# Kernel tuning notes

Measured on AMD Instinct MI355X. Metric: run time of the kernel, lower is better.

The kernel has to match this reference:

```python
import jax, jax.numpy as jnp
import numpy as np

B, N, SEM, STR = 64, 512, 256, 256  # batch, tokens, sem_dim_size, str_dim_size (hidden=512)


def setup_inputs() -> dict:
    key = jax.random.key(0)
    ks = jax.random.split(key, 8)
    s = 0.02  # small init so exp(f_ij)/exp(f_i) stay well-conditioned
    return {
        "input": jax.random.normal(ks[0], (B, N, SEM + STR), jnp.float32),
        "Wp": (jax.random.normal(ks[1], (STR, STR), jnp.float32) * s),
        "bp": jnp.zeros((STR,), jnp.float32),
        "Wbil": (jax.random.normal(ks[2], (STR, STR), jnp.float32) * s),
        "bbil": jnp.zeros((), jnp.float32),
        "Wfi": (jax.random.normal(ks[3], (1, STR), jnp.float32) * s),
        "bfi": jnp.zeros((1,), jnp.float32),
        "exparam": jax.random.normal(ks[4], (1, 1, SEM), jnp.float32),
        "Wfz": (jax.random.normal(ks[5], (SEM, 2 * SEM), jnp.float32) * s),
        "bfz": jnp.zeros((SEM,), jnp.float32),
    }


def reference(input, Wp, bp, Wbil, bbil, Wfi, bfi, exparam, Wfz, bfz):
    b, n, _ = input.shape
    sem_v = input[:, :, :SEM]          # [B,N,SEM]
    str_v = input[:, :, SEM:]          # [B,N,STR]

    # NOTE: source uses tp_linear for BOTH tp and tc, and expands both with
    # unsqueeze(2), so f_ij[b,i,j] = bilinear(tp[b,i], tp[b,i]) is constant in j.
    tp = str_v @ Wp.T + bp             # [B,N,STR]
    s = jnp.einsum('bid,de,bie->bi', tp, Wbil, tp) + bbil   # [B,N]
    f_ij = jnp.broadcast_to(s[:, :, None], (b, n, n))        # [B,N,N]

    f_i = jnp.exp(str_v @ Wfi.T + bfi)[..., 0]               # [B,N]

    off = 1.0 - jnp.eye(n, dtype=input.dtype)
    A = jnp.exp(f_ij) * off                                  # zero diagonal
    deg = jnp.sum(A, axis=2)                                 # [B,N]
    L = -A + deg[:, :, None] * jnp.eye(n, dtype=input.dtype) # Laplacian
    L = L.at[:, 0, :].set(f_i)                               # root-augmented L_bar

    LLinv = jnp.linalg.inv(L)                                # [B,N,N]
    d0 = f_i * LLinv[:, :, 0]                                # root marginals [B,N]
    dg = jnp.diagonal(LLinv, axis1=-2, axis2=-1)             # [B,N]

    # tmp1 and tmp2 in the source both reduce to A[b,i,j] * diag[b,j]
    tmp = A * dg[:, None, :]
    mask1 = jnp.concatenate([jnp.zeros((n, 1)), jnp.ones((n, n - 1))], 1).astype(input.dtype)
    mask2 = jnp.concatenate([jnp.zeros((1, n)), jnp.ones((n - 1, n))], 0).astype(input.dtype)
    dx = (mask1 - mask2) * tmp                               # [B,N,N]

    d = jnp.concatenate([d0[:, None, :], dx], axis=1)        # [B,N+1,N]
    df = jnp.swapaxes(d, 1, 2)                               # [B,N,N+1]
    ssr = jnp.concatenate([jnp.broadcast_to(exparam, (b, 1, SEM)), sem_v], 1)  # [B,N+1,SEM]
    pinp = jnp.einsum('bnm,bmd->bnd', df, ssr)               # [B,N,SEM]
    # cinp = dx @ sem_v is computed in the source but never used -> omitted

    finp = jnp.concatenate([sem_v, pinp], axis=-1)           # [B,N,2*SEM]
    return jax.nn.relu(finp @ Wfz.T + bfz)                   # [B,N,SEM]
```

## Files before the change

### kernel.cpp

```cpp
#include <hip/hip_runtime.h>
#include <math.h>

#define B_    64
#define N_    512
#define SEM_  256
#define STR_  256
#define DIM_  512
#define ROWS_ (B_*N_)

#define OFF_T      0
#define OFF_QT16   65536
#define OFF_W116   98304
#define OFF_W2T    131072
#define OFF_V1     196608
#define OFF_C1     196864
#define OFF_H      197120
#define OFF_C0     197376
#define OFF_EV     197440
#define OFF_FV     230208
#define OFF_SUMP   262976
#define OFF_V2B    394048
#define OFF_ROW0   410432

typedef __bf16 bf16x8 __attribute__((ext_vector_type(8)));
typedef float  f32x4  __attribute__((ext_vector_type(4)));

__device__ __forceinline__ ushort f2b(float x) {
    return __builtin_bit_cast(ushort, (__bf16)x);
}
__device__ __forceinline__ float b2f(ushort h) {
    unsigned u = ((unsigned)h) << 16;
    return __builtin_bit_cast(float, u);
}
__device__ __forceinline__ float bflo(unsigned u) {
    return __builtin_bit_cast(float, u << 16);
}
__device__ __forceinline__ float bfhi(unsigned u) {
    return __builtin_bit_cast(float, u & 0xffff0000u);
}

__global__ __launch_bounds__(256) void k0a(
    const float* __restrict__ Wp, const float* __restrict__ bp,
    const float* __restrict__ Wbil, const float* __restrict__ Wfz,
    const float* __restrict__ exparam,
    float* __restrict__ T, ushort* __restrict__ W116, float* __restrict__ W2t,
    float* __restrict__ v1, float* __restrict__ h, float* __restrict__ c0)
{
    int t = threadIdx.x, a = blockIdx.x;
    float acc = 0.f;
    const float* wb = Wbil + a*256;
    for (int c = 0; c < 256; ++c) acc += wb[c] * Wp[c*256 + t];
    T[a*256 + t] = acc;
    W116[a*256 + t] = f2b(Wfz[a*512 + t]);
    W2t[t*256 + a] = Wfz[a*512 + 256 + t];
    if (a == 0) {
        float s = 0.f;
        const float* w2 = Wfz + t*512 + 256;
        for (int dd = 0; dd < 256; ++dd) s += w2[dd] * exparam[dd];
        v1[t] = s;
    }
    if (a == 1) {
        float g = 0.f, g2 = 0.f;
        for (int c = 0; c < 256; ++c) {
            g  += Wbil[t*256 + c] * bp[c];
            g2 += Wbil[c*256 + t] * bp[c];
        }
        h[t] = g + g2;
        __shared__ float red[256];
        red[t] = bp[t] * g;
        __syncthreads();
        for (int s2 = 128; s2 > 0; s2 >>= 1) {
            if (t < s2) red[t] += red[t + s2];
            __syncthreads();
        }
        if (t == 0) c0[0] = red[0];
    }
}

__global__ __launch_bounds__(256) void k0b(
    const float* __restrict__ Wp, const float* __restrict__ T,
    const float* __restrict__ h,
    ushort* __restrict__ Qt16, float* __restrict__ c1)
{
    int t = threadIdx.x, d = blockIdx.x;
    float acc = 0.f;
    for (int a2 = 0; a2 < 256; ++a2) acc += Wp[a2*256 + d] * T[a2*256 + t];
    Qt16[t*256 + d] = f2b(acc);
    __shared__ float red[256];
    red[t] = Wp[t*256 + d] * h[t];
    __syncthreads();
    for (int s2 = 128; s2 > 0; s2 >>= 1) {
        if (t < s2) red[t] += red[t + s2];
        __syncthreads();
    }
    if (t == 0) c1[d] = red[0];
}

__global__ __launch_bounds__(256) void k_rowstats(
    const float* __restrict__ input, const ushort* __restrict__ Qt16,
    const float* __restrict__ c1, const float* __restrict__ c0,
    const float* __restrict__ Wfi, const float* __restrict__ bbil,
    const float* __restrict__ bfi, const float* __restrict__ W2t,
    float* __restrict__ Ev, float* __restrict__ fv, float* __restrict__ v2b)
{
    __shared__ __align__(16) char smem[69632];
    ushort* Ash   = (ushort*)smem;
    ushort* Bsm   = (ushort*)(smem + 32768);
    ushort* Ush   = (ushort*)(smem + 32768);
    float*  sdiag = (float*)(smem + 65536);
    float*  fdiag = (float*)(smem + 66560);
    float*  s0sh  = (float*)(smem + 67584);
    float*  shE0  = (float*)(smem + 68608);

    int t = threadIdx.x;
    int lane = t & 63, w = t >> 6;
    int g = lane >> 4, li = lane & 15;
    long rowbase = (long)blockIdx.x * 64;
    int b = (int)(rowbase >> 9);
    int i0 = (int)(rowbase & 511);
    const float* Ab = input + rowbase*DIM_ + SEM_;

#pragma unroll
    for (int q = 0; q < 16; ++q) {
        int v = t + 256*q;
        int r = v >> 6, c4 = v & 63;
        float4 a4 = *(const float4*)(Ab + (long)r*DIM_ + c4*4);
        ushort4 b4 = make_ushort4(f2b(a4.x), f2b(a4.y), f2b(a4.z), f2b(a4.w));
        *(ushort4*)&Ash[r*256 + ((c4*4) ^ ((r & 7) << 3))] = b4;
    }

    f32x4 acc[4][4];
#pragma unroll
    for (int m = 0; m < 4; ++m)
#pragma unroll
        for (int n = 0; n < 4; ++n) acc[m][n] = (f32x4){0.f, 0.f, 0.f, 0.f};

    for (int k0 = 0; k0 < 256; k0 += 32) {
#pragma unroll
        for (int q = 0; q < 4; ++q) {
            int v = t + 256*q;
            int n = v >> 2, c = v & 3;
            *(uint4*)&Bsm[n*40 + c*8] = *(const uint4*)&Qt16[n*256 + k0 + c*8];
        }
        __syncthreads();
        bf16x8 af[4], bfr[4];
        int xs = (li & 7) << 3;
#pragma unroll
        for (int m = 0; m < 4; ++m)
            af[m] = *(const bf16x8*)&Ash[(m*16 + li)*256 + ((k0 + g*8) ^ xs)];
#pragma unroll
        for (int n = 0; n < 4; ++n)
            bfr[n] = *(const bf16x8*)&Bsm[(w*64 + n*16 + li)*40 + g*8];
#pragma unroll
        for (int m = 0; m < 4; ++m)
#pragma unroll
            for (int n = 0; n < 4; ++n)
                acc[m][n] = __builtin_amdgcn_mfma_f32_16x16x32_bf16(af[m], bfr[n], acc[m][n], 0, 0, 0);
        __syncthreads();
    }

    float c1v[4];
#pragma unroll
    for (int n = 0; n < 4; ++n) c1v[n] = c1[w*64 + n*16 + li];
#pragma unroll
    for (int m = 0; m < 4; ++m)
#pragma unroll
        for (int n = 0; n < 4; ++n)
#pragma unroll
            for (int reg = 0; reg < 4; ++reg) {
                int row = m*16 + g*4 + reg;
                int col = w*64 + n*16 + li;
                Ush[row*256 + (col ^ ((row & 7) << 3))] = f2b(acc[m][n][reg] + c1v[n]);
            }
    __syncthreads();

    f32x4 dacc[4], facc[4];
#pragma unroll
    for (int m = 0; m < 4; ++m) { dacc[m] = (f32x4){0.f,0.f,0.f,0.f}; facc[m] = (f32x4){0.f,0.f,0.f,0.f}; }
#pragma unroll
    for (int kk = 0; kk < 2; ++kk) {
        int kb = (w*2 + kk)*32 + g*8;
        float4 wf0 = *(const float4*)(Wfi + kb);
        float4 wf1 = *(const float4*)(Wfi + kb + 4);
        bf16x8 afw = (bf16x8){(__bf16)wf0.x, (__bf16)wf0.y, (__bf16)wf0.z, (__bf16)wf0.w,
                              (__bf16)wf1.x, (__bf16)wf1.y, (__bf16)wf1.z, (__bf16)wf1.w};
        int xs = (li & 7) << 3;
#pragma unroll
        for (int m = 0; m < 4; ++m) {
            int ridx = (m*16 + li)*256 + (kb ^ xs);
            bf16x8 afu = *(const bf16x8*)&Ush[ridx];
            bf16x8 bfs = *(const bf16x8*)&Ash[ridx];
            dacc[m] = __builtin_amdgcn_mfma_f32_16x16x32_bf16(afu, bfs, dacc[m], 0, 0, 0);
            facc[m] = __builtin_amdgcn_mfma_f32_16x16x32_bf16(afw, bfs, facc[m], 0, 0, 0);
        }
    }
    if (g == (li >> 2)) {
        int dr = li & 3;
#pragma unroll
        for (int m = 0; m < 4; ++m) {
            float dv = dr == 0 ? dacc[m][0] : dr == 1 ? dacc[m][1] : dr == 2 ? dacc[m][2] : dacc[m][3];
            sdiag[(m*16 + li)*4 + w] = dv;
        }
    }
    if (g == 0) {
#pragma unroll
        for (int m = 0; m < 4; ++m) fdiag[(m*16 + li)*4 + w] = facc[m][0];
    }
    __syncthreads();
    if (t < 64) {
        float ss = sdiag[t*4] + sdiag[t*4+1] + sdiag[t*4+2] + sdiag[t*4+3];
        float ff = fdiag[t*4] + fdiag[t*4+1] + fdiag[t*4+2] + fdiag[t*4+3];
        float ev = expf(ss + c0[0] + bbil[0]);
        Ev[rowbase + t] = ev;
        fv[rowbase + t] = expf(ff + bfi[0]);
        if (t == 0) shE0[0] = ev;
    }

    if (i0 == 0) {
        if (t < 64)
            *(float4*)&s0sh[t*4] = *(const float4*)(input + (long)b*512*DIM_ + t*4);
        __syncthreads();
        float a2 = 0.f;
        for (int d = 0; d < 256; ++d) a2 += W2t[d*256 + t] * s0sh[d];
        v2b[b*256 + t] = shE0[0] * a2;
    }
}

__global__ __launch_bounds__(256) void k_final(
    const float* __restrict__ input, const ushort* __restrict__ W116,
    const float* __restrict__ v1, const float* __restrict__ v2b,
    const float* __restrict__ Ev, const float* __restrict__ fv,
    const float* __restrict__ bfz,
    float* __restrict__ sump, float* __restrict__ row0pre,
    float* __restrict__ out)
{
    __shared__ __align__(16) char smem[62976];
    ushort* Ash    = (ushort*)smem;
    ushort* Bsm    = (ushort*)(smem + 32768);
    float*  Csh    = (float*)smem;
    float*  sumred = (float*)(smem + 53248);
    float*  cAs    = (float*)(smem + 61440);
    float*  cBs    = (float*)(smem + 61696);
    float*  EvL    = (float*)(smem + 61952);
    float*  wred   = (float*)(smem + 62208);

    int t = threadIdx.x;
    int lane = t & 63, w = t >> 6;
    int g = lane >> 4, li = lane & 15;
    long rowbase = (long)blockIdx.x * 64;
    int b = (int)(rowbase >> 9);
    int i0 = (int)(rowbase & 511);
    const float* Ab = input + rowbase*DIM_;

    float fsum = fv[b*512 + t] + fv[b*512 + 256 + t];
#pragma unroll
    for (int off = 32; off >= 1; off >>= 1) fsum += __shfl_down(fsum, off);
    if (lane == 0) wred[w] = fsum;
    __syncthreads();
    float invF = 1.0f / (wred[0] + wred[1] + wred[2] + wred[3]);

    if (t < 64) {
        int row = (int)rowbase + t;
        float fr = fv[row];
        float ev = Ev[row];
        EvL[t] = (i0 == 0 && t == 0) ? 0.f : ev;
        cAs[t] = fr * invF;
        cBs[t] = ((i0 + t) == 0) ? -invF
               : (1.0f + (fv[b*512] - fr)*invF) / (512.0f * ev);
    }

#pragma unroll
    for (int q = 0; q < 16; ++q) {
        int v = t + 256*q;
        int r = v >> 6, c4 = v & 63;
        float4 a4 = *(const float4*)(Ab + (long)r*DIM_ + c4*4);
        ushort4 b4 = make_ushort4(f2b(a4.x), f2b(a4.y), f2b(a4.z), f2b(a4.w));
        *(ushort4*)&Ash[r*256 + ((c4*4) ^ ((r & 7) << 3))] = b4;
    }

    f32x4 acc[4][4];
#pragma unroll
    for (int m = 0; m < 4; ++m)
#pragma unroll
        for (int n = 0; n < 4; ++n) acc[m][n] = (f32x4){0.f, 0.f, 0.f, 0.f};

    for (int k0 = 0; k0 < 256; k0 += 32) {
#pragma unroll
        for (int q = 0; q < 4; ++q) {
            int v = t + 256*q;
            int n = v >> 2, c = v & 3;
            *(uint4*)&Bsm[n*40 + c*8] = *(const uint4*)&W116[n*256 + k0 + c*8];
        }
        __syncthreads();
        bf16x8 af[4], bfr[4];
        int xs = (li & 7) << 3;
#pragma unroll
        for (int m = 0; m < 4; ++m)
            af[m] = *(const bf16x8*)&Ash[(m*16 + li)*256 + ((k0 + g*8) ^ xs)];
#pragma unroll
        for (int n = 0; n < 4; ++n)
            bfr[n] = *(const bf16x8*)&Bsm[(w*64 + n*16 + li)*40 + g*8];
#pragma unroll
        for (int m = 0; m < 4; ++m)
#pragma unroll
            for (int n = 0; n < 4; ++n)
                acc[m][n] = __builtin_amdgcn_mfma_f32_16x16x32_bf16(af[m], bfr[n], acc[m][n], 0, 0, 0);
        __syncthreads();
    }

    {
        int qq = t >> 5, c8 = t & 31;
        float p[8];
#pragma unroll
        for (int i = 0; i < 8; ++i) p[i] = 0.f;
#pragma unroll
        for (int rr = 0; rr < 8; ++rr) {
            int r = qq*8 + rr;
            float ev = EvL[r];
            uint4 uv = *(const uint4*)&Ash[r*256 + ((c8*8) ^ (rr << 3))];
            p[0] += ev * bflo(uv.x); p[1] += ev * bfhi(uv.x);
            p[2] += ev * bflo(uv.y); p[3] += ev * bfhi(uv.y);
            p[4] += ev * bflo(uv.z); p[5] += ev * bfhi(uv.z);
            p[6] += ev * bflo(uv.w); p[7] += ev * bfhi(uv.w);
        }
        *(float4*)&sumred[qq*256 + c8*8]     = (float4){p[0], p[1], p[2], p[3]};
        *(float4*)&sumred[qq*256 + c8*8 + 4] = (float4){p[4], p[5], p[6], p[7]};
    }
    __syncthreads();
    {
        float sp = 0.f;
#pragma unroll
        for (int qq = 0; qq < 8; ++qq) sp += sumred[qq*256 + t];
        sump[(long)blockIdx.x*256 + t] = sp;
    }

    float v1v[4], v2v[4], bzv[4];
#pragma unroll
    for (int n = 0; n < 4; ++n) {
        int col = w*64 + n*16 + li;
        v1v[n] = v1[col];
        v2v[n] = v2b[b*256 + col];
        bzv[n] = bfz[col];
    }

#pragma unroll
    for (int hh = 0; hh < 2; ++hh) {
        __syncthreads();
#pragma unroll
        for (int mm = 0; mm < 2; ++mm) {
            int m = hh*2 + mm;
#pragma unroll
            for (int reg = 0; reg < 4; ++reg) {
                int row = m*16 + g*4 + reg;
                float ca = cAs[row], cb = cBs[row];
                int irow = i0 + row;
#pragma unroll
                for (int n = 0; n < 4; ++n) {
                    int col = w*64 + n*16 + li;
                    float sel = (irow == 0) ? 0.f : v2v[n];
                    float val = acc[m][n][reg] + ca*v1v[n] + cb*sel + bzv[n];
                    if (irow == 0) row0pre[b*256 + col] = val;
                    Csh[(row - hh*32)*264 + col] = fmaxf(val, 0.f);
                }
            }
        }
        __syncthreads();
#pragma unroll
        for (int q = 0; q < 8; ++q) {
            int v = t + 256*q;
            int r = v >> 6, c4 = v & 63;
            *(float4*)(out + (rowbase + hh*32 + r)*256 + c4*4) = *(const float4*)&Csh[r*264 + c4*4];
        }
    }
}

__global__ __launch_bounds__(256) void k_fix(
    const float* __restrict__ sump, const float* __restrict__ fv,
    const float* __restrict__ W2t, const float* __restrict__ row0pre,
    float* __restrict__ out)
{
    int b = blockIdx.x, t = threadIdx.x;
    __shared__ float svsh[256];
    __shared__ float redF[256];
    float a = 0.f;
#pragma unroll
    for (int p = 0; p < 8; ++p) a += sump[(long)(b*8 + p)*256 + t];
    svsh[t] = a;
    redF[t] = fv[b*512 + t] + fv[b*512 + 256 + t];
    __syncthreads();
    for (int s2 = 128; s2 > 0; s2 >>= 1) {
        if (t < s2) redF[t] += redF[t + s2];
        __syncthreads();
    }
    float invF = 1.0f / redF[0];
    float a0 = 0.f;
    for (int d = 0; d < 256; ++d) a0 += W2t[d*256 + t] * svsh[d];
    out[((long)b*512)*256 + t] = fmaxf(row0pre[b*256 + t] - invF*a0, 0.f);
}

extern "C" void kernel_launch(void* const* d_in, const int* in_sizes, int n_in,
                              void* d_out, int out_size, void* d_ws, size_t ws_size,
                              hipStream_t stream) {
    const float* input   = (const float*)d_in[0];
    const float* Wp      = (const float*)d_in[1];
    const float* bp      = (const float*)d_in[2];
    const float* Wbil    = (const float*)d_in[3];
    const float* bbil    = (const float*)d_in[4];
    const float* Wfi     = (const float*)d_in[5];
    const float* bfi     = (const float*)d_in[6];
    const float* exparam = (const float*)d_in[7];
    const float* Wfz     = (const float*)d_in[8];
    const float* bfz     = (const float*)d_in[9];
    float* ws  = (float*)d_ws;
    float* out = (float*)d_out;

    float*  T     = ws + OFF_T;
    ushort* Qt16  = (ushort*)(ws + OFF_QT16);
    ushort* W116  = (ushort*)(ws + OFF_W116);
    float*  W2t   = ws + OFF_W2T;
    float*  v1    = ws + OFF_V1;
    float*  c1    = ws + OFF_C1;
    float*  h     = ws + OFF_H;
    float*  c0    = ws + OFF_C0;
    float*  Ev    = ws + OFF_EV;
    float*  fv    = ws + OFF_FV;
    float*  sump  = ws + OFF_SUMP;
    float*  v2b   = ws + OFF_V2B;
    float*  row0p = ws + OFF_ROW0;

    k0a<<<256, 256, 0, stream>>>(Wp, bp, Wbil, Wfz, exparam, T, W116, W2t, v1, h, c0);
    k0b<<<256, 256, 0, stream>>>(Wp, T, h, Qt16, c1);
    k_rowstats<<<ROWS_/64, 256, 0, stream>>>(input, Qt16, c1, c0, Wfi, bbil, bfi, W2t, Ev, fv, v2b);
    k_final<<<ROWS_/64, 256, 0, stream>>>(input, W116, v1, v2b, Ev, fv, bfz, sump, row0p, out);
    k_fix<<<B_, 256, 0, stream>>>(sump, fv, W2t, row0p, out);
}
```

Baseline: 88.98 us.

## Load GEMM B operands straight from global and shrink LDS for higher occupancy

Both GEMM kernels stop staging the bf16 weight tiles in shared memory and instead load B fragments directly from global memory/L2 into registers each k-step, removing per-iteration barriers. The Ush staging in k_rowstats is split into two 128-column halves, and k_final's output buffer uses an XOR swizzle instead of padding, cutting LDS use so three blocks can fit per CU (launch_bounds 256,3). This trades LDS traffic and syncs for uncoalesced-ish global reads of weights and higher register pressure.

Result: slower. 93.50 us (+5.1%).

```diff
diff --git a/kernel.cpp b/kernel.cpp
--- a/kernel.cpp
+++ b/kernel.cpp
@@ -27,10 +27,6 @@
 
 __device__ __forceinline__ ushort f2b(float x) {
     return __builtin_bit_cast(ushort, (__bf16)x);
-}
-__device__ __forceinline__ float b2f(ushort h) {
-    unsigned u = ((unsigned)h) << 16;
-    return __builtin_bit_cast(float, u);
 }
 __device__ __forceinline__ float bflo(unsigned u) {
     return __builtin_bit_cast(float, u << 16);
@@ -96,21 +92,20 @@
     if (t == 0) c1[d] = red[0];
 }
 
-__global__ __launch_bounds__(256) void k_rowstats(
+__global__ __launch_bounds__(256, 3) void k_rowstats(
     const float* __restrict__ input, const ushort* __restrict__ Qt16,
     const float* __restrict__ c1, const float* __restrict__ c0,
     const float* __restrict__ Wfi, const float* __restrict__ bbil,
     const float* __restrict__ bfi, const float* __restrict__ W2t,
     float* __restrict__ Ev, float* __restrict__ fv, float* __restrict__ v2b)
 {
-    __shared__ __align__(16) char smem[69632];
+    __shared__ __align__(16) char smem[52288];
     ushort* Ash   = (ushort*)smem;
-    ushort* Bsm   = (ushort*)(smem + 32768);
     ushort* Ush   = (ushort*)(smem + 32768);
-    float*  sdiag = (float*)(smem + 65536);
-    float*  fdiag = (float*)(smem + 66560);
-    float*  s0sh  = (float*)(smem + 67584);
-    float*  shE0  = (float*)(smem + 68608);
+    float*  sdiag = (float*)(smem + 49152);
+    float*  fdiag = (float*)(smem + 50176);
+    float*  s0sh  = (float*)(smem + 51200);
+    float*  shE0  = (float*)(smem + 52224);
 
     int t = threadIdx.x;
     int lane = t & 63, w = t >> 6;
@@ -128,6 +123,7 @@
         ushort4 b4 = make_ushort4(f2b(a4.x), f2b(a4.y), f2b(a4.z), f2b(a4.w));
         *(ushort4*)&Ash[r*256 + ((c4*4) ^ ((r & 7) << 3))] = b4;
     }
+    __syncthreads();
 
     f32x4 acc[4][4];
 #pragma unroll
@@ -135,65 +131,63 @@
 #pragma unroll
         for (int n = 0; n < 4; ++n) acc[m][n] = (f32x4){0.f, 0.f, 0.f, 0.f};
 
+    int xs = (li & 7) << 3;
+#pragma unroll 2
     for (int k0 = 0; k0 < 256; k0 += 32) {
-#pragma unroll
-        for (int q = 0; q < 4; ++q) {
-            int v = t + 256*q;
-            int n = v >> 2, c = v & 3;
-            *(uint4*)&Bsm[n*40 + c*8] = *(const uint4*)&Qt16[n*256 + k0 + c*8];
-        }
-        __syncthreads();
         bf16x8 af[4], bfr[4];
-        int xs = (li & 7) << 3;
+#pragma unroll
+        for (int n = 0; n < 4; ++n)
+            bfr[n] = *(const bf16x8*)&Qt16[(w*64 + n*16 + li)*256 + k0 + g*8];
 #pragma unroll
         for (int m = 0; m < 4; ++m)
             af[m] = *(const bf16x8*)&Ash[(m*16 + li)*256 + ((k0 + g*8) ^ xs)];
 #pragma unroll
-        for (int n = 0; n < 4; ++n)
-            bfr[n] = *(const bf16x8*)&Bsm[(w*64 + n*16 + li)*40 + g*8];
-#pragma unroll
         for (int m = 0; m < 4; ++m)
 #pragma unroll
             for (int n = 0; n < 4; ++n)
                 acc[m][n] = __builtin_amdgcn_mfma_f32_16x16x32_bf16(af[m], bfr[n], acc[m][n], 0, 0, 0);
-        __syncthreads();
     }
 
     float c1v[4];
 #pragma unroll
     for (int n = 0; n < 4; ++n) c1v[n] = c1[w*64 + n*16 + li];
-#pragma unroll
-    for (int m = 0; m < 4; ++m)
-#pragma unroll
-        for (int n = 0; n < 4; ++n)
-#pragma unroll
-            for (int reg = 0; reg < 4; ++reg) {
-                int row = m*16 + g*4 + reg;
-                int col = w*64 + n*16 + li;
-                Ush[row*256 + (col ^ ((row & 7) << 3))] = f2b(acc[m][n][reg] + c1v[n]);
-            }
-    __syncthreads();
 
     f32x4 dacc[4], facc[4];
 #pragma unroll
     for (int m = 0; m < 4; ++m) { dacc[m] = (f32x4){0.f,0.f,0.f,0.f}; facc[m] = (f32x4){0.f,0.f,0.f,0.f}; }
-#pragma unroll
-    for (int kk = 0; kk < 2; ++kk) {
-        int kb = (w*2 + kk)*32 + g*8;
-        float4 wf0 = *(const float4*)(Wfi + kb);
-        float4 wf1 = *(const float4*)(Wfi + kb + 4);
+
+#pragma unroll
+    for (int h = 0; h < 2; ++h) {
+        if ((w >> 1) == h) {
+            int cl0 = (w & 1)*64;
+#pragma unroll
+            for (int m = 0; m < 4; ++m)
+#pragma unroll
+                for (int n = 0; n < 4; ++n)
+#pragma unroll
+                    for (int reg = 0; reg < 4; ++reg) {
+                        int row = m*16 + g*4 + reg;
+                        int cl = cl0 + n*16 + li;
+                        Ush[row*128 + (cl ^ ((row & 7) << 3))] = f2b(acc[m][n][reg] + c1v[n]);
+                    }
+        }
+        __syncthreads();
+        int kb = w*32 + g*8;
+        int kg = h*128 + kb;
+        float4 wf0 = *(const float4*)(Wfi + kg);
+        float4 wf1 = *(const float4*)(Wfi + kg + 4);
         bf16x8 afw = (bf16x8){(__bf16)wf0.x, (__bf16)wf0.y, (__bf16)wf0.z, (__bf16)wf0.w,
                               (__bf16)wf1.x, (__bf16)wf1.y, (__bf16)wf1.z, (__bf16)wf1.w};
-        int xs = (li & 7) << 3;
 #pragma unroll
         for (int m = 0; m < 4; ++m) {
-            int ridx = (m*16 + li)*256 + (kb ^ xs);
-            bf16x8 afu = *(const bf16x8*)&Ush[ridx];
-            bf16x8 bfs = *(const bf16x8*)&Ash[ridx];
+            bf16x8 afu = *(const bf16x8*)&Ush[(m*16 + li)*128 + (kb ^ xs)];
+            bf16x8 bfs = *(const bf16x8*)&Ash[(m*16 + li)*256 + (kg ^ xs)];
             dacc[m] = __builtin_amdgcn_mfma_f32_16x16x32_bf16(afu, bfs, dacc[m], 0, 0, 0);
             facc[m] = __builtin_amdgcn_mfma_f32_16x16x32_bf16(afw, bfs, facc[m], 0, 0, 0);
         }
-    }
+        __syncthreads();
+    }
+
     if (g == (li >> 2)) {
         int dr = li & 3;
 #pragma unroll
@@ -226,7 +220,7 @@
     }
 }
 
-__global__ __launch_bounds__(256) void k_final(
+__global__ __launch_bounds__(256, 3) void k_final(
     const float* __restrict__ input, const ushort* __restrict__ W116,
     const float* __restrict__ v1, const float* __restrict__ v2b,
     const float* __restrict__ Ev, const float* __restrict__ fv,
@@ -234,15 +228,14 @@
     float* __restrict__ sump, float* __restrict__ row0pre,
     float* __restrict__ out)
 {
-    __shared__ __align__(16) char smem[62976];
+    __shared__ __align__(16) char smem[41792];
     ushort* Ash    = (ushort*)smem;
-    ushort* Bsm    = (ushort*)(smem + 32768);
     float*  Csh    = (float*)smem;
-    float*  sumred = (float*)(smem + 53248);
-    float*  cAs    = (float*)(smem + 61440);
-    float*  cBs    = (float*)(smem + 61696);
-    float*  EvL    = (float*)(smem + 61952);
-    float*  wred   = (float*)(smem + 62208);
+    float*  sumred = (float*)(smem + 32768);
+    float*  cAs    = (float*)(smem + 40960);
+    float*  cBs    = (float*)(smem + 41216);
+    float*  EvL    = (float*)(smem + 41472);
+    float*  wred   = (float*)(smem + 41728);
 
     int t = threadIdx.x;
     int lane = t & 63, w = t >> 6;
@@ -277,6 +270,7 @@
         ushort4 b4 = make_ushort4(f2b(a4.x), f2b(a4.y), f2b(a4.z), f2b(a4.w));
         *(ushort4*)&Ash[r*256 + ((c4*4) ^ ((r & 7) << 3))] = b4;
     }
+    __syncthreads();
 
     f32x4 acc[4][4];
 #pragma unroll
@@ -284,28 +278,21 @@
 #pragma unroll
         for (int n = 0; n < 4; ++n) acc[m][n] = (f32x4){0.f, 0.f, 0.f, 0.f};
 
+    int xs = (li & 7) << 3;
+#pragma unroll 2
     for (int k0 = 0; k0 < 256; k0 += 32) {
-#pragma unroll
-        for (int q = 0; q < 4; ++q) {
-            int v = t + 256*q;
-            int n = v >> 2, c = v & 3;
-            *(uint4*)&Bsm[n*40 + c*8] = *(const uint4*)&W116[n*256 + k0 + c*8];
-        }
-        __syncthreads();
         bf16x8 af[4], bfr[4];
-        int xs = (li & 7) << 3;
+#pragma unroll
+        for (int n = 0; n < 4; ++n)
+            bfr[n] = *(const bf16x8*)&W116[(w*64 + n*16 + li)*256 + k0 + g*8];
 #pragma unroll
         for (int m = 0; m < 4; ++m)
             af[m] = *(const bf16x8*)&Ash[(m*16 + li)*256 + ((k0 + g*8) ^ xs)];
 #pragma unroll
-        for (int n = 0; n < 4; ++n)
-            bfr[n] = *(const bf16x8*)&Bsm[(w*64 + n*16 + li)*40 + g*8];
-#pragma unroll
         for (int m = 0; m < 4; ++m)
 #pragma unroll
             for (int n = 0; n < 4; ++n)
                 acc[m][n] = __builtin_amdgcn_mfma_f32_16x16x32_bf16(af[m], bfr[n], acc[m][n], 0, 0, 0);
-        __syncthreads();
     }
 
     {
@@ -352,6 +339,8 @@
 #pragma unroll
             for (int reg = 0; reg < 4; ++reg) {
                 int row = m*16 + g*4 + reg;
+                int row_l = row - hh*32;
+                int sw = ((row_l >> 2) & 3) << 3;
                 float ca = cAs[row], cb = cBs[row];
                 int irow = i0 + row;
 #pragma unroll
@@ -360,7 +349,7 @@
                     float sel = (irow == 0) ? 0.f : v2v[n];
                     float val = acc[m][n][reg] + ca*v1v[n] + cb*sel + bzv[n];
                     if (irow == 0) row0pre[b*256 + col] = val;
-                    Csh[(row - hh*32)*264 + col] = fmaxf(val, 0.f);
+                    Csh[row_l*256 + (col ^ sw)] = fmaxf(val, 0.f);
                 }
             }
         }
@@ -369,7 +358,9 @@
         for (int q = 0; q < 8; ++q) {
             int v = t + 256*q;
             int r = v >> 6, c4 = v & 63;
-            *(float4*)(out + (rowbase + hh*32 + r)*256 + c4*4) = *(const float4*)&Csh[r*264 + c4*4];
+            int sw = ((r >> 2) & 3) << 3;
+            *(float4*)(out + (rowbase + hh*32 + r)*256 + c4*4) =
+                *(const float4*)&Csh[r*256 + ((c4*4) ^ sw)];
         }
     }
 }
```

## Load GEMM B-fragments directly from global, drop LDS staging and per-step barriers

Applied to the files above, without the earlier changes.

In the two MFMA GEMM kernels, the B operand (Qt16 / W116 weights) is now read straight from global memory into registers instead of being staged through shared memory with two barriers per k-step. This removes the LDS round-trip and synchronisation inside the k loop and relies on L1/L2 caching of the small shared weight matrix. The k0b setup kernel is also reindexed so its global reads coalesce, and several scalar reduction loops get unroll pragmas. Uncoalesced 16-byte global loads per lane could add latency in exchange.

Measured after the change: 106.8 us. 20.0% more time.

```diff
diff --git a/kernel.cpp b/kernel.cpp
--- a/kernel.cpp
+++ b/kernel.cpp
@@ -28,10 +28,6 @@
 __device__ __forceinline__ ushort f2b(float x) {
     return __builtin_bit_cast(ushort, (__bf16)x);
 }
-__device__ __forceinline__ float b2f(ushort h) {
-    unsigned u = ((unsigned)h) << 16;
-    return __builtin_bit_cast(float, u);
-}
 __device__ __forceinline__ float bflo(unsigned u) {
     return __builtin_bit_cast(float, u << 16);
 }
@@ -49,6 +45,7 @@
     int t = threadIdx.x, a = blockIdx.x;
     float acc = 0.f;
     const float* wb = Wbil + a*256;
+#pragma unroll 16
     for (int c = 0; c < 256; ++c) acc += wb[c] * Wp[c*256 + t];
     T[a*256 + t] = acc;
     W116[a*256 + t] = f2b(Wfz[a*512 + t]);
@@ -56,11 +53,13 @@
     if (a == 0) {
         float s = 0.f;
         const float* w2 = Wfz + t*512 + 256;
+#pragma unroll 16
         for (int dd = 0; dd < 256; ++dd) s += w2[dd] * exparam[dd];
         v1[t] = s;
     }
     if (a == 1) {
         float g = 0.f, g2 = 0.f;
+#pragma unroll 8
         for (int c = 0; c < 256; ++c) {
             g  += Wbil[t*256 + c] * bp[c];
             g2 += Wbil[c*256 + t] * bp[c];
@@ -82,18 +81,19 @@
     const float* __restrict__ h,
     ushort* __restrict__ Qt16, float* __restrict__ c1)
 {
-    int t = threadIdx.x, d = blockIdx.x;
+    int t = threadIdx.x, e = blockIdx.x;
     float acc = 0.f;
-    for (int a2 = 0; a2 < 256; ++a2) acc += Wp[a2*256 + d] * T[a2*256 + t];
-    Qt16[t*256 + d] = f2b(acc);
+#pragma unroll 16
+    for (int a2 = 0; a2 < 256; ++a2) acc += Wp[a2*256 + t] * T[a2*256 + e];
+    Qt16[e*256 + t] = f2b(acc);
     __shared__ float red[256];
-    red[t] = Wp[t*256 + d] * h[t];
+    red[t] = Wp[t*256 + e] * h[t];
     __syncthreads();
     for (int s2 = 128; s2 > 0; s2 >>= 1) {
         if (t < s2) red[t] += red[t + s2];
         __syncthreads();
     }
-    if (t == 0) c1[d] = red[0];
+    if (t == 0) c1[e] = red[0];
 }
 
 __global__ __launch_bounds__(256) void k_rowstats(
@@ -105,7 +105,6 @@
 {
     __shared__ __align__(16) char smem[69632];
     ushort* Ash   = (ushort*)smem;
-    ushort* Bsm   = (ushort*)(smem + 32768);
     ushort* Ush   = (ushort*)(smem + 32768);
     float*  sdiag = (float*)(smem + 65536);
     float*  fdiag = (float*)(smem + 66560);
@@ -119,6 +118,7 @@
     int b = (int)(rowbase >> 9);
     int i0 = (int)(rowbase & 511);
     const float* Ab = input + rowbase*DIM_ + SEM_;
+    int xs = (li & 7) << 3;
 
 #pragma unroll
     for (int q = 0; q < 16; ++q) {
@@ -128,6 +128,7 @@
         ushort4 b4 = make_ushort4(f2b(a4.x), f2b(a4.y), f2b(a4.z), f2b(a4.w));
         *(ushort4*)&Ash[r*256 + ((c4*4) ^ ((r & 7) << 3))] = b4;
     }
+    __syncthreads();
 
     f32x4 acc[4][4];
 #pragma unroll
@@ -135,28 +136,20 @@
 #pragma unroll
         for (int n = 0; n < 4; ++n) acc[m][n] = (f32x4){0.f, 0.f, 0.f, 0.f};
 
+#pragma unroll 4
     for (int k0 = 0; k0 < 256; k0 += 32) {
-#pragma unroll
-        for (int q = 0; q < 4; ++q) {
-            int v = t + 256*q;
-            int n = v >> 2, c = v & 3;
-            *(uint4*)&Bsm[n*40 + c*8] = *(const uint4*)&Qt16[n*256 + k0 + c*8];
-        }
-        __syncthreads();
         bf16x8 af[4], bfr[4];
-        int xs = (li & 7) << 3;
+#pragma unroll
+        for (int n = 0; n < 4; ++n)
+            bfr[n] = *(const bf16x8*)&Qt16[(w*64 + n*16 + li)*256 + k0 + g*8];
 #pragma unroll
         for (int m = 0; m < 4; ++m)
             af[m] = *(const bf16x8*)&Ash[(m*16 + li)*256 + ((k0 + g*8) ^ xs)];
 #pragma unroll
-        for (int n = 0; n < 4; ++n)
-            bfr[n] = *(const bf16x8*)&Bsm[(w*64 + n*16 + li)*40 + g*8];
-#pragma unroll
         for (int m = 0; m < 4; ++m)
 #pragma unroll
             for (int n = 0; n < 4; ++n)
                 acc[m][n] = __builtin_amdgcn_mfma_f32_16x16x32_bf16(af[m], bfr[n], acc[m][n], 0, 0, 0);
-        __syncthreads();
     }
 
     float c1v[4];
@@ -184,7 +177,6 @@
         float4 wf1 = *(const float4*)(Wfi + kb + 4);
         bf16x8 afw = (bf16x8){(__bf16)wf0.x, (__bf16)wf0.y, (__bf16)wf0.z, (__bf16)wf0.w,
                               (__bf16)wf1.x, (__bf16)wf1.y, (__bf16)wf1.z, (__bf16)wf1.w};
-        int xs = (li & 7) << 3;
 #pragma unroll
         for (int m = 0; m < 4; ++m) {
             int ridx = (m*16 + li)*256 + (kb ^ xs);
@@ -221,6 +213,7 @@
             *(float4*)&s0sh[t*4] = *(const float4*)(input + (long)b*512*DIM_ + t*4);
         __syncthreads();
         float a2 = 0.f;
+#pragma unroll 8
         for (int d = 0; d < 256; ++d) a2 += W2t[d*256 + t] * s0sh[d];
         v2b[b*256 + t] = shE0[0] * a2;
     }
@@ -236,7 +229,6 @@
 {
     __shared__ __align__(16) char smem[62976];
     ushort* Ash    = (ushort*)smem;
-    ushort* Bsm    = (ushort*)(smem + 32768);
     float*  Csh    = (float*)smem;
     float*  sumred = (float*)(smem + 53248);
     float*  cAs    = (float*)(smem + 61440);
@@ -251,6 +243,7 @@
     int b = (int)(rowbase >> 9);
     int i0 = (int)(rowbase & 511);
     const float* Ab = input + rowbase*DIM_;
+    int xs = (li & 7) << 3;
 
     float fsum = fv[b*512 + t] + fv[b*512 + 256 + t];
 #pragma unroll
@@ -277,6 +270,7 @@
         ushort4 b4 = make_ushort4(f2b(a4.x), f2b(a4.y), f2b(a4.z), f2b(a4.w));
         *(ushort4*)&Ash[r*256 + ((c4*4) ^ ((r & 7) << 3))] = b4;
     }
+    __syncthreads();
 
     f32x4 acc[4][4];
 #pragma unroll
@@ -284,28 +278,20 @@
 #pragma unroll
         for (int n = 0; n < 4; ++n) acc[m][n] = (f32x4){0.f, 0.f, 0.f, 0.f};
 
+#pragma unroll 4
     for (int k0 = 0; k0 < 256; k0 += 32) {
-#pragma unroll
-        for (int q = 0; q < 4; ++q) {
-            int v = t + 256*q;
-            int n = v >> 2, c = v & 3;
-            *(uint4*)&Bsm[n*40 + c*8] = *(const uint4*)&W116[n*256 + k0 + c*8];
-        }
-        __syncthreads();
         bf16x8 af[4], bfr[4];
-        int xs = (li & 7) << 3;
+#pragma unroll
+        for (int n = 0; n < 4; ++n)
+            bfr[n] = *(const bf16x8*)&W116[(w*64 + n*16 + li)*256 + k0 + g*8];
 #pragma unroll
         for (int m = 0; m < 4; ++m)
             af[m] = *(const bf16x8*)&Ash[(m*16 + li)*256 + ((k0 + g*8) ^ xs)];
 #pragma unroll
-        for (int n = 0; n < 4; ++n)
-            bfr[n] = *(const bf16x8*)&Bsm[(w*64 + n*16 + li)*40 + g*8];
-#pragma unroll
         for (int m = 0; m < 4; ++m)
 #pragma unroll
             for (int n = 0; n < 4; ++n)
                 acc[m][n] = __builtin_amdgcn_mfma_f32_16x16x32_bf16(af[m], bfr[n], acc[m][n], 0, 0, 0);
-        __syncthreads();
     }
 
     {
@@ -394,6 +380,7 @@
     }
     float invF = 1.0f / redF[0];
     float a0 = 0.f;
+#pragma unroll 8
     for (int d = 0; d < 256; ++d) a0 += W2t[d*256 + t] * svsh[d];
     out[((long)b*512)*256 + t] = fmaxf(row0pre[b*256 + t] - invF*a0, 0.f);
 }
```
